# Kernel optimization log

Measured on AMD Instinct MI355X. Metric: run time of the kernel, lower is better.

Reference implementation:

```python
import jax, jax.numpy as jnp
import numpy as np

B, S, D, H, HD, E, DE = 2, 512, 768, 12, 64, 50, 50  # batch, seq, input_dim, heads, head_dim, edge_dim, dep_embed_dim


def setup_inputs() -> dict:
    key = jax.random.key(0)
    ks = jax.random.split(key, 16)
    def xn(k, shape, s=0.02):
        return (jax.random.normal(k, shape, jnp.float32) * s)
    return {
        'weight_prob_softmax': jax.random.uniform(ks[0], (B, S, S, E), jnp.float32),
        'weight_adj': jax.random.normal(ks[1], (B, S, S, E), jnp.float32),
        'gcn_inputs': jax.random.normal(ks[2], (B, S, D), jnp.float32),
        'self_loop': jax.random.uniform(ks[3], (B, S, S, E), jnp.float32),
        # self.linear
        'W_lin': xn(ks[4], (D, D)), 'b_lin': jnp.zeros((D,), jnp.float32),
        # additive attention vectors fc_w1 / fc_w2 (stored [H, HD])
        'fc_w1': xn(ks[5], (H, HD), 0.2), 'fc_w2': xn(ks[6], (H, HD), 0.2),
        # edge_mlp: Linear(E,128) -> ReLU -> (Dropout eval) -> Linear(128,H)
        'We1': xn(ks[7], (128, E), 0.1), 'be1': jnp.zeros((128,), jnp.float32),
        'We2': xn(ks[8], (H, 128), 0.1), 'be2': jnp.zeros((H,), jnp.float32),
        # self.W output projection
        'W_out': xn(ks[9], (D, D)), 'b_out': jnp.zeros((D,), jnp.float32),
        # LayerNorm params
        'ln_a': jnp.ones((D,), jnp.float32), 'ln_b': jnp.zeros((D,), jnp.float32),
        # highway.W split into column blocks: [edge | edge_i | edge_j | node1 | node2]
        'Wh_e': xn(ks[10], (DE, E), 0.1), 'Wh_ei': xn(ks[11], (DE, E), 0.1),
        'Wh_ej': xn(ks[12], (DE, E), 0.1), 'Wh_n1': xn(ks[13], (DE, D), 0.05),
        'Wh_n2': xn(ks[14], (DE, D), 0.05), 'bh': jnp.zeros((DE,), jnp.float32),
    }


def reference(weight_prob_softmax, weight_adj, gcn_inputs, self_loop,
              W_lin, b_lin, fc_w1, fc_w2, We1, be1, We2, be2,
              W_out, b_out, ln_a, ln_b, Wh_e, Wh_ei, Wh_ej, Wh_n1, Wh_n2, bh):
    wps = self_loop + weight_prob_softmax                      # [B,S,S,E]
    mask = jnp.sum(wps, axis=-1) == 0.0                        # [B,S,S]
    feature = (gcn_inputs @ W_lin.T + b_lin).reshape(B, S, H, HD)
    attn_src = jnp.einsum('bshd,hd->bhs', feature, fc_w1)      # [B,H,S]
    attn_dst = jnp.einsum('bshd,hd->bhs', feature, fc_w2)      # [B,H,S]
    # edge MLP bias (dropout is identity in eval)
    hmid = jax.nn.relu(jnp.einsum('bije,fe->bijf', wps, We1) + be1)  # [B,S,S,128]
    A = jnp.einsum('bijf,hf->bhij', hmid, We2) + be2[None, :, None, None]  # [B,H,S,S]
    attn = jax.nn.leaky_relu(attn_src[:, :, :, None] + attn_dst[:, :, None, :] + A,
                             negative_slope=0.01)
    attn = jnp.where(mask[:, None, :, :], -jnp.inf, attn)
    attn = jax.nn.softmax(attn, axis=-1)
    gcn = jnp.einsum('bhij,bjhd->bihd', attn, feature).reshape(B, S, D)
    gcn = gcn @ W_out.T + b_out
    # torch LayerNorm variant: unbiased std, divide by (std + eps)
    mean = jnp.mean(gcn, axis=-1, keepdims=True)
    std = jnp.std(gcn, axis=-1, ddof=1, keepdims=True)
    gcn = ln_a * (gcn - mean) / (std + 1e-6) + ln_b
    node = jax.nn.relu(gcn)                                    # [B,S,D]
    # RefiningStrategy: W([edge, edge_i, edge_j, node1, node2]) via block matmuls
    ediag = jnp.diagonal(weight_adj, axis1=1, axis2=2).transpose(0, 2, 1)  # [B,S,E]
    edge_out = (jnp.einsum('bije,fe->bijf', weight_adj, Wh_e)
                + (ediag @ Wh_ei.T)[:, :, None, :]             # edge_i[b,i,j]=diag[b,i]
                + (ediag @ Wh_ej.T)[:, None, :, :]             # edge_j[b,i,j]=diag[b,j]
                + (node @ Wh_n1.T)[:, None, :, :]              # node1[b,i,j]=node[b,j]
                + (node @ Wh_n2.T)[:, :, None, :]              # node2[b,i,j]=node[b,i]
                + bh)                                          # [B,S,S,DE]
    return node, edge_out
```

## Files before the change

kernel.cpp:

```cpp
#include <hip/hip_runtime.h>
#include <math.h>
#include <stddef.h>

#define BB 2
#define SS 512
#define DD 768
#define HH 12
#define HDIM 64
#define EE 50
#define DE 50
#define F1 128

typedef float f32x4 __attribute__((ext_vector_type(4)));
typedef short s16x8 __attribute__((ext_vector_type(8)));

static __device__ __forceinline__ unsigned short f2bf(float x) {
  unsigned int u = __float_as_uint(x);
  unsigned int r = u + 0x7fffu + ((u >> 16) & 1u);
  return (unsigned short)(r >> 16);
}
static __device__ __forceinline__ float bf2f(unsigned short b) {
  return __uint_as_float(((unsigned int)b) << 16);
}

__global__ __launch_bounds__(256) void k_gemm_bias(
    const float* __restrict__ X, int ldx,
    const float* __restrict__ W,
    const float* __restrict__ bias,
    float* __restrict__ Y, int ldy,
    int M, int N, int K)
{
  __shared__ float Xs[32][68];
  __shared__ float Ws[32][68];
  int t = threadIdx.x;
  int tx = t & 15, ty = t >> 4;
  int m0 = blockIdx.y * 64, n0 = blockIdx.x * 64;
  float acc[4][4] = {};
  for (int k0 = 0; k0 < K; k0 += 32) {
#pragma unroll
    for (int q = 0; q < 2; ++q) {
      int idx = t + q * 256;
      int r = idx >> 3, c = (idx & 7) << 2;
      float4 v = *(const float4*)(X + (size_t)(m0 + r) * ldx + k0 + c);
      Xs[c + 0][r] = v.x; Xs[c + 1][r] = v.y; Xs[c + 2][r] = v.z; Xs[c + 3][r] = v.w;
      float4 w = *(const float4*)(W + (size_t)(n0 + r) * K + k0 + c);
      Ws[c + 0][r] = w.x; Ws[c + 1][r] = w.y; Ws[c + 2][r] = w.z; Ws[c + 3][r] = w.w;
    }
    __syncthreads();
#pragma unroll
    for (int kk = 0; kk < 32; ++kk) {
      float a[4], b[4];
#pragma unroll
      for (int u = 0; u < 4; ++u) a[u] = Xs[kk][ty * 4 + u];
#pragma unroll
      for (int u = 0; u < 4; ++u) b[u] = Ws[kk][tx * 4 + u];
#pragma unroll
      for (int i = 0; i < 4; ++i)
#pragma unroll
        for (int j = 0; j < 4; ++j) acc[i][j] += a[i] * b[j];
    }
    __syncthreads();
  }
#pragma unroll
  for (int i = 0; i < 4; ++i) {
    int m = m0 + ty * 4 + i;
#pragma unroll
    for (int j = 0; j < 4; ++j) {
      int n = n0 + tx * 4 + j;
      Y[(size_t)m * ldy + n] = acc[i][j] + bias[n];
    }
  }
}

__global__ __launch_bounds__(192) void k_attnvec(
    const float* __restrict__ feat, const float* __restrict__ w1,
    const float* __restrict__ w2, float* __restrict__ src, float* __restrict__ dst)
{
  int bs = blockIdx.x;
  int t = threadIdx.x;
  int h = t >> 4, l = t & 15;
  float4 f = *(const float4*)(feat + (size_t)bs * DD + h * HDIM + l * 4);
  float4 a = *(const float4*)(w1 + h * HDIM + l * 4);
  float4 c = *(const float4*)(w2 + h * HDIM + l * 4);
  float ps = f.x * a.x + f.y * a.y + f.z * a.z + f.w * a.w;
  float pd = f.x * c.x + f.y * c.y + f.z * c.z + f.w * c.w;
#pragma unroll
  for (int o = 8; o > 0; o >>= 1) {
    ps += __shfl_xor(ps, o);
    pd += __shfl_xor(pd, o);
  }
  if (l == 0) {
    int b = bs >> 9, s = bs & 511;
    src[((b * HH + h) << 9) + s] = ps;
    dst[((b * HH + h) << 9) + s] = pd;
  }
}

__global__ __launch_bounds__(64) void k_prep(
    const float* __restrict__ We1, const float* __restrict__ be1,
    const float* __restrict__ We2, const float* __restrict__ Whe,
    s16x8* __restrict__ wtab, float* __restrict__ betab,
    s16x8* __restrict__ wtabE)
{
  const int l = threadIdx.x;
  const int lr = l & 15, lg = l >> 4;
#pragma unroll
  for (int ks = 0; ks < 2; ++ks)
#pragma unroll
    for (int n = 0; n < 8; ++n) {
      s16x8 v;
#pragma unroll
      for (int u = 0; u < 8; ++u) {
        int e = ks * 32 + lg * 8 + u;
        float x = (e < 50) ? We1[(n * 16 + lr) * 50 + e] : 0.0f;
        v[u] = (short)f2bf(x);
      }
      wtab[(ks * 8 + n) * 64 + l] = v;
    }
#pragma unroll
  for (int kk = 0; kk < 4; ++kk) {
    s16x8 v;
#pragma unroll
    for (int u = 0; u < 8; ++u) {
      int f = kk * 32 + lg * 8 + u;
      v[u] = (short)((lr < 12) ? f2bf(We2[lr * 128 + f]) : (unsigned short)0);
    }
    wtab[(16 + kk) * 64 + l] = v;
  }
#pragma unroll
  for (int n = 0; n < 8; ++n) betab[n * 64 + l] = be1[n * 16 + lr];
#pragma unroll
  for (int nt = 0; nt < 4; ++nt)
#pragma unroll
    for (int ks = 0; ks < 2; ++ks) {
      int f = nt * 16 + lr;
      s16x8 v;
#pragma unroll
      for (int u = 0; u < 8; ++u) {
        int e = ks * 32 + lg * 8 + u;
        float x = (f < 50 && e < 50) ? Whe[f * 50 + e] : 0.0f;
        v[u] = (short)f2bf(x);
      }
      wtabE[(nt * 2 + ks) * 64 + l] = v;
    }
}

__global__ __launch_bounds__(256, 4) void k_scores_mfma(
    const float* __restrict__ wprob, const float* __restrict__ sloop,
    const s16x8* __restrict__ wtab, const float* __restrict__ betab,
    const float* __restrict__ be2,
    const float* __restrict__ src, const float* __restrict__ dst,
    float* __restrict__ scores)
{
  __shared__ unsigned short wps_s[128][72];
  __shared__ unsigned short hmid_s[128][72];
  __shared__ float masks[128];

  const int blk = blockIdx.x;
  const int c = blk & 3;
  const int i = (blk >> 2) & 511;
  const int b = blk >> 11;
  const int j0c = c << 7;
  const int t = threadIdx.x;
  const int w = t >> 6, l = t & 63;
  const int lr = l & 15, lg = l >> 4;
  const int jbase = w * 32;

  const size_t rowbase = (size_t)(b * SS + i) * SS * EE + (size_t)c * 6400;
  float4 pw[7], psl[7];
  {
    const float* wp = wprob + rowbase;
    const float* sl = sloop + rowbase;
#pragma unroll
    for (int k = 0; k < 7; ++k)
      if (k < 6 || t < 64) {
        pw[k] = *(const float4*)(wp + 4 * (t + 256 * k));
        psl[k] = *(const float4*)(sl + 4 * (t + 256 * k));
      }
  }

  s16x8 wb[4];
#pragma unroll
  for (int kk = 0; kk < 4; ++kk) wb[kk] = wtab[(16 + kk) * 64 + l];
  float be1v[8];
#pragma unroll
  for (int n = 0; n < 8; ++n) be1v[n] = betab[n * 64 + l];
  const int hc = (lr < 12) ? lr : 0;
  const float be2v = be2[hc];
  const float srcv = src[((b * HH + hc) << 9) + i];
  const float* drow = dst + ((size_t)(b * HH + hc) << 9);
  float4 dv0 = *(const float4*)(drow + j0c + jbase + lg * 4);
  float4 dv1 = *(const float4*)(drow + j0c + jbase + 16 + lg * 4);

  for (int q = t; q < 896; q += 256) {
    int r = q / 7, cd = 25 + q % 7;
    ((unsigned int*)wps_s)[r * 36 + cd] = 0u;
  }

#pragma unroll
  for (int k = 0; k < 7; ++k)
    if (k < 6 || t < 64) {
      int f = 4 * (t + 256 * k);
      int j = f / 50;
      int e0 = f - j * 50;
      float vs[4] = {pw[k].x + psl[k].x, pw[k].y + psl[k].y,
                     pw[k].z + psl[k].z, pw[k].w + psl[k].w};
#pragma unroll
      for (int u = 0; u < 4; ++u) {
        int e = e0 + u, jj = j;
        if (e >= 50) { e -= 50; jj += 1; }
        wps_s[jj][e] = f2bf(vs[u]);
      }
    }
  __syncthreads();

  if (l < 32) {
    const unsigned short* row = wps_s[jbase + l];
    float s = 0.0f;
#pragma unroll
    for (int q = 0; q < 6; ++q) {
      s16x8 v = *(const s16x8*)(row + q * 8);
#pragma unroll
      for (int u = 0; u < 8; ++u) s += bf2f((unsigned short)v[u]);
    }
    unsigned int last = *(const unsigned int*)(row + 48);
    s += bf2f((unsigned short)(last & 0xffffu)) + bf2f((unsigned short)(last >> 16));
    masks[jbase + l] = (s == 0.0f) ? 1.0f : 0.0f;
  }

  s16x8 aA[2][2];
#pragma unroll
  for (int ks = 0; ks < 2; ++ks) {
    aA[0][ks] = *(const s16x8*)&wps_s[jbase + lr][ks * 32 + lg * 8];
    aA[1][ks] = *(const s16x8*)&wps_s[jbase + 16 + lr][ks * 32 + lg * 8];
  }

  f32x4 accB[2] = {};
#pragma unroll
  for (int h = 0; h < 2; ++h) {
    s16x8 wah[2][4];
#pragma unroll
    for (int ks = 0; ks < 2; ++ks)
#pragma unroll
      for (int nn = 0; nn < 4; ++nn)
        wah[ks][nn] = wtab[(ks * 8 + h * 4 + nn) * 64 + l];

    f32x4 accA[2][4] = {};
#pragma unroll
    for (int ks = 0; ks < 2; ++ks)
#pragma unroll
      for (int nn = 0; nn < 4; ++nn) {
        accA[0][nn] = __builtin_amdgcn_mfma_f32_16x16x32_bf16(aA[0][ks], wah[ks][nn], accA[0][nn], 0, 0, 0);
        accA[1][nn] = __builtin_amdgcn_mfma_f32_16x16x32_bf16(aA[1][ks], wah[ks][nn], accA[1][nn], 0, 0, 0);
      }
#pragma unroll
    for (int jt = 0; jt < 2; ++jt)
#pragma unroll
      for (int nn = 0; nn < 4; ++nn)
#pragma unroll
        for (int r = 0; r < 4; ++r) {
          float v = fmaxf(accA[jt][nn][r] + be1v[h * 4 + nn], 0.0f);
          hmid_s[jbase + jt * 16 + lg * 4 + r][nn * 16 + lr] = f2bf(v);
        }

#pragma unroll
    for (int kh = 0; kh < 2; ++kh) {
      int kk = 2 * h + kh;
      s16x8 a0 = *(const s16x8*)&hmid_s[jbase + lr][kh * 32 + lg * 8];
      s16x8 a1 = *(const s16x8*)&hmid_s[jbase + 16 + lr][kh * 32 + lg * 8];
      accB[0] = __builtin_amdgcn_mfma_f32_16x16x32_bf16(a0, wb[kk], accB[0], 0, 0, 0);
      accB[1] = __builtin_amdgcn_mfma_f32_16x16x32_bf16(a1, wb[kk], accB[1], 0, 0, 0);
    }
  }

  if (lr < 12) {
#pragma unroll
    for (int jt = 0; jt < 2; ++jt) {
      int jl = jbase + jt * 16 + lg * 4;
      const float4 dv = jt ? dv1 : dv0;
      float4 st;
#pragma unroll
      for (int r = 0; r < 4; ++r) {
        float x = accB[jt][r] + be2v + srcv + (&dv.x)[r];
        x = (x > 0.0f) ? x : 0.01f * x;
        if (masks[jl + r] != 0.0f) x = -INFINITY;
        (&st.x)[r] = x;
      }
      *(float4*)(scores + ((((size_t)(b * SS + i)) * HH + lr) << 9) + j0c + jl) = st;
    }
  }
}

__global__ __launch_bounds__(256) void k_softmax_pv(
    const float* __restrict__ scores, const float* __restrict__ feat,
    float* __restrict__ gout)
{
  __shared__ float p[2][12][512];
  int blk = blockIdx.x;
  int b = blk >> 8;
  int i0 = (blk & 255) << 1;
  int t = threadIdx.x;
  size_t base = ((size_t)(b * SS + i0) * HH) << 9;
  for (int q = t; q < 12288; q += 256) ((float*)p)[q] = scores[base + q];
  __syncthreads();

  int w = t >> 6, l = t & 63;
  for (int r = w; r < 24; r += 4) {
    int ii = r / 12, h = r % 12;
    float* row = p[ii][h];
    float vv[8];
    float m = -INFINITY;
#pragma unroll
    for (int u = 0; u < 8; ++u) {
      vv[u] = row[l + (u << 6)];
      m = fmaxf(m, vv[u]);
    }
#pragma unroll
    for (int o = 32; o > 0; o >>= 1) m = fmaxf(m, __shfl_xor(m, o));
    float s = 0.0f;
#pragma unroll
    for (int u = 0; u < 8; ++u) {
      float e = __expf(vv[u] - m);
      vv[u] = e;
      s += e;
    }
#pragma unroll
    for (int o = 32; o > 0; o >>= 1) s += __shfl_xor(s, o);
    float inv = 1.0f / s;
#pragma unroll
    for (int u = 0; u < 8; ++u) row[l + (u << 6)] = vv[u] * inv;
  }
  __syncthreads();

  float acc[2][3] = {};
  const float* fb = feat + (size_t)b * SS * DD;
  int h0 = t >> 6;
#pragma unroll 4
  for (int j = 0; j < 512; ++j) {
    const float* fr = fb + (size_t)j * DD;
    float f0 = fr[t], f1 = fr[t + 256], f2 = fr[t + 512];
    float p00 = p[0][h0][j], p10 = p[1][h0][j];
    float p01 = p[0][h0 + 4][j], p11 = p[1][h0 + 4][j];
    float p02 = p[0][h0 + 8][j], p12 = p[1][h0 + 8][j];
    acc[0][0] += p00 * f0; acc[0][1] += p01 * f1; acc[0][2] += p02 * f2;
    acc[1][0] += p10 * f0; acc[1][1] += p11 * f1; acc[1][2] += p12 * f2;
  }
#pragma unroll
  for (int ii = 0; ii < 2; ++ii)
#pragma unroll
    for (int u = 0; u < 3; ++u)
      gout[(size_t)(b * SS + i0 + ii) * DD + t + (u << 8)] = acc[ii][u];
}

__global__ __launch_bounds__(256) void k_ln(
    const float* __restrict__ gcn2, const float* __restrict__ ga,
    const float* __restrict__ gb, float* __restrict__ out)
{
  __shared__ float rs[4], rss[4];
  int row = blockIdx.x;
  int t = threadIdx.x;
  const float* x = gcn2 + (size_t)row * DD;
  float v[3];
  float s = 0.0f, ss2 = 0.0f;
#pragma unroll
  for (int u = 0; u < 3; ++u) {
    v[u] = x[t + (u << 8)];
    s += v[u];
    ss2 += v[u] * v[u];
  }
#pragma unroll
  for (int o = 32; o > 0; o >>= 1) {
    s += __shfl_down(s, o);
    ss2 += __shfl_down(ss2, o);
  }
  int w = t >> 6, l = t & 63;
  if (l == 0) { rs[w] = s; rss[w] = ss2; }
  __syncthreads();
  float S = rs[0] + rs[1] + rs[2] + rs[3];
  float SSum = rss[0] + rss[1] + rss[2] + rss[3];
  float mean = S * (1.0f / 768.0f);
  float var = (SSum - 768.0f * mean * mean) * (1.0f / 767.0f);
  var = fmaxf(var, 0.0f);
  float rinv = 1.0f / (sqrtf(var) + 1e-6f);
#pragma unroll
  for (int u = 0; u < 3; ++u) {
    int cidx = t + (u << 8);
    float y = ga[cidx] * (v[u] - mean) * rinv + gb[cidx];
    out[(size_t)row * DD + cidx] = fmaxf(y, 0.0f);
  }
}

__global__ __launch_bounds__(256) void k_pq(
    const float* __restrict__ node, const float* __restrict__ wadj,
    const float* __restrict__ Whei, const float* __restrict__ Whej,
    const float* __restrict__ Whn1, const float* __restrict__ Whn2,
    const float* __restrict__ bh, float* __restrict__ P, float* __restrict__ Q)
{
  __shared__ float nd[2][768];
  __shared__ float ed[2][64];
  const int bs0 = blockIdx.x * 2;
  const int t = threadIdx.x;
  const int w = t >> 6, l = t & 63;

  for (int q = t; q < 384; q += 256) {
    int rr = q / 192, idx = q % 192;
    *(float4*)(nd[rr] + idx * 4) =
        *(const float4*)(node + (size_t)(bs0 + rr) * DD + idx * 4);
  }
  {
    int rr = t >> 7, tt = t & 127;
    if (tt < 50) {
      int bs = bs0 + rr;
      int b = bs >> 9, s = bs & 511;
      ed[rr][tt] = wadj[((size_t)(b * SS + s) * SS + s) * EE + tt];
    }
  }
  __syncthreads();

  float4 n00 = *(const float4*)(nd[0] + l * 4);
  float4 n01 = *(const float4*)(nd[0] + 256 + l * 4);
  float4 n02 = *(const float4*)(nd[0] + 512 + l * 4);
  float4 n10 = *(const float4*)(nd[1] + l * 4);
  float4 n11 = *(const float4*)(nd[1] + 256 + l * 4);
  float4 n12 = *(const float4*)(nd[1] + 512 + l * 4);
  float el0 = (l < 50) ? ed[0][l] : 0.0f;
  float el1 = (l < 50) ? ed[1][l] : 0.0f;

  for (int o = w; o < 100; o += 4) {
    const int which = (o >= 50);
    const int f = o - which * 50;
    const float* Wn = which ? Whn1 : Whn2;
    const float* We = which ? Whej : Whei;
    const float* wr = Wn + f * DD;
    float4 w0 = *(const float4*)(wr + l * 4);
    float4 w1 = *(const float4*)(wr + 256 + l * 4);
    float4 w2 = *(const float4*)(wr + 512 + l * 4);
    float wev = (l < 50) ? We[f * EE + l] : 0.0f;
    float a0 = n00.x * w0.x + n00.y * w0.y + n00.z * w0.z + n00.w * w0.w
             + n01.x * w1.x + n01.y * w1.y + n01.z * w1.z + n01.w * w1.w
             + n02.x * w2.x + n02.y * w2.y + n02.z * w2.z + n02.w * w2.w
             + el0 * wev;
    float a1 = n10.x * w0.x + n10.y * w0.y + n10.z * w0.z + n10.w * w0.w
             + n11.x * w1.x + n11.y * w1.y + n11.z * w1.z + n11.w * w1.w
             + n12.x * w2.x + n12.y * w2.y + n12.z * w2.z + n12.w * w2.w
             + el1 * wev;
#pragma unroll
    for (int ofs = 32; ofs > 0; ofs >>= 1) {
      a0 += __shfl_xor(a0, ofs);
      a1 += __shfl_xor(a1, ofs);
    }
    if (l == 0) {
      float bias = which ? bh[f] : 0.0f;
      float* dst0 = (which ? Q : P) + (size_t)bs0 * DE + f;
      dst0[0] = a0 + bias;
      dst0[DE] = a1 + bias;
    }
  }
}

__global__ __launch_bounds__(256) void k_edge_mfma(
    const float* __restrict__ wadj, const s16x8* __restrict__ wtabE,
    const float* __restrict__ P, const float* __restrict__ Q,
    float* __restrict__ eout)
{
  __shared__ __align__(16) unsigned char raw[25600];
  unsigned short (*adj_s)[72] = (unsigned short(*)[72])raw;
  float* park = (float*)raw;
  __shared__ float P_s[64];

  const int t = threadIdx.x;
  const size_t n0 = (size_t)blockIdx.x * 128;
  const int b = (int)(n0 >> 18);
  const int i = (int)((n0 & 262143) >> 9);
  const int j0 = (int)(n0 & 511);
  const int w = t >> 6, l = t & 63;
  const int lr = l & 15, lg = l >> 4;
  const int mbase = w * 32;

  float4 pw[7];
  {
    const float* wp = wadj + n0 * EE;
#pragma unroll
    for (int k = 0; k < 7; ++k)
      if (k < 6 || t < 64) pw[k] = *(const float4*)(wp + 4 * (t + 256 * k));
  }

  s16x8 we[4][2];
#pragma unroll
  for (int nt = 0; nt < 4; ++nt)
#pragma unroll
    for (int ks = 0; ks < 2; ++ks) we[nt][ks] = wtabE[(nt * 2 + ks) * 64 + l];
  if (t < 64) P_s[t] = (t < 50) ? P[(size_t)(b * SS + i) * DE + t] : 0.0f;

  for (int q = t; q < 896; q += 256) {
    int r = q / 7, cd = 25 + q % 7;
    ((unsigned int*)adj_s)[r * 36 + cd] = 0u;
  }

#pragma unroll
  for (int k = 0; k < 7; ++k)
    if (k < 6 || t < 64) {
      int f = 4 * (t + 256 * k);
      int j = f / 50;
      int e0 = f - j * 50;
#pragma unroll
      for (int u = 0; u < 4; ++u) {
        int e = e0 + u, jj = j;
        if (e >= 50) { e -= 50; jj += 1; }
        adj_s[jj][e] = f2bf((&pw[k].x)[u]);
      }
    }
  __syncthreads();

  f32x4 acc[2][4] = {};
#pragma unroll
  for (int ks = 0; ks < 2; ++ks) {
    s16x8 a0 = *(const s16x8*)&adj_s[mbase + lr][ks * 32 + lg * 8];
    s16x8 a1 = *(const s16x8*)&adj_s[mbase + 16 + lr][ks * 32 + lg * 8];
#pragma unroll
    for (int nt = 0; nt < 4; ++nt) {
      acc[0][nt] = __builtin_amdgcn_mfma_f32_16x16x32_bf16(a0, we[nt][ks], acc[0][nt], 0, 0, 0);
      acc[1][nt] = __builtin_amdgcn_mfma_f32_16x16x32_bf16(a1, we[nt][ks], acc[1][nt], 0, 0, 0);
    }
  }
  __syncthreads();

#pragma unroll
  for (int nt = 0; nt < 4; ++nt) {
    int f = nt * 16 + lr;
    if (f < 50) {
      float pf = P_s[f];
#pragma unroll
      for (int mt = 0; mt < 2; ++mt) {
        int m = mbase + mt * 16 + lg * 4;
        const float* qp = Q + (size_t)(b * SS + j0 + m) * DE + f;
#pragma unroll
        for (int r = 0; r < 4; ++r)
          park[(m + r) * DE + f] = acc[mt][nt][r] + pf + qp[r * DE];
      }
    }
  }
  __syncthreads();

  const float4* s4 = (const float4*)park;
  float4* d4 = (float4*)(eout + n0 * DE);
  for (int q = t; q < 1600; q += 256) d4[q] = s4[q];
}

extern "C" void kernel_launch(void* const* d_in, const int* in_sizes, int n_in,
                              void* d_out, int out_size, void* d_ws, size_t ws_size,
                              hipStream_t stream)
{
  const float* wprob = (const float*)d_in[0];
  const float* wadj  = (const float*)d_in[1];
  const float* gin   = (const float*)d_in[2];
  const float* sloop = (const float*)d_in[3];
  const float* W_lin = (const float*)d_in[4];
  const float* b_lin = (const float*)d_in[5];
  const float* fw1   = (const float*)d_in[6];
  const float* fw2   = (const float*)d_in[7];
  const float* We1   = (const float*)d_in[8];
  const float* be1   = (const float*)d_in[9];
  const float* We2   = (const float*)d_in[10];
  const float* be2   = (const float*)d_in[11];
  const float* W_out = (const float*)d_in[12];
  const float* b_out = (const float*)d_in[13];
  const float* ln_a  = (const float*)d_in[14];
  const float* ln_b  = (const float*)d_in[15];
  const float* Whe   = (const float*)d_in[16];
  const float* Whei  = (const float*)d_in[17];
  const float* Whej  = (const float*)d_in[18];
  const float* Whn1  = (const float*)d_in[19];
  const float* Whn2  = (const float*)d_in[20];
  const float* bh    = (const float*)d_in[21];

  float* ws = (float*)d_ws;
  float* feature = ws + 0;
  float* src     = ws + 786432;
  float* dst     = ws + 798720;
  float* scores  = ws + 811008;
  float* gcnmid  = ws + 7102464;
  float* gcn2    = ws + 7888896;
  float* P       = ws + 8675328;
  float* Q       = ws + 8726528;
  s16x8* wtab    = (s16x8*)(ws + 8777728);
  float* betab   = ws + 8782848;
  s16x8* wtabE   = (s16x8*)(ws + 8783360);

  float* node = (float*)d_out;
  float* eout = (float*)d_out + 786432;

  k_prep<<<1, 64, 0, stream>>>(We1, be1, We2, Whe, wtab, betab, wtabE);
  k_gemm_bias<<<dim3(DD / 64, (BB * SS) / 64), 256, 0, stream>>>(
      gin, DD, W_lin, b_lin, feature, DD, BB * SS, DD, DD);
  k_attnvec<<<BB * SS, 192, 0, stream>>>(feature, fw1, fw2, src, dst);
  k_scores_mfma<<<BB * SS * 4, 256, 0, stream>>>(
      wprob, sloop, wtab, betab, be2, src, dst, scores);
  k_softmax_pv<<<BB * SS / 2, 256, 0, stream>>>(scores, feature, gcnmid);
  k_gemm_bias<<<dim3(DD / 64, (BB * SS) / 64), 256, 0, stream>>>(
      gcnmid, DD, W_out, b_out, gcn2, DD, BB * SS, DD, DD);
  k_ln<<<BB * SS, 256, 0, stream>>>(gcn2, ln_a, ln_b, node);
  k_pq<<<BB * SS / 2, 256, 0, stream>>>(node, wadj, Whei, Whej, Whn1, Whn2, bh, P, Q);
  k_edge_mfma<<<(BB * SS * SS) / 128, 256, 0, stream>>>(wadj, wtabE, P, Q, eout);
}
```

Baseline: 284.2 us.

## Split scores kernel into single-wave blocks with shared LDS buffer and no barrier

```diff
diff --git a/kernel.cpp b/kernel.cpp
--- a/kernel.cpp
+++ b/kernel.cpp
@@ -145,37 +145,34 @@
     }
 }
 
-__global__ __launch_bounds__(256, 4) void k_scores_mfma(
+__global__ __launch_bounds__(64, 6) void k_scores_mfma(
     const float* __restrict__ wprob, const float* __restrict__ sloop,
     const s16x8* __restrict__ wtab, const float* __restrict__ betab,
     const float* __restrict__ be2,
     const float* __restrict__ src, const float* __restrict__ dst,
     float* __restrict__ scores)
 {
-  __shared__ unsigned short wps_s[128][72];
-  __shared__ unsigned short hmid_s[128][72];
-  __shared__ float masks[128];
+  __shared__ unsigned short buf[32][72];
+  __shared__ float masks[32];
 
   const int blk = blockIdx.x;
-  const int c = blk & 3;
-  const int i = (blk >> 2) & 511;
-  const int b = blk >> 11;
-  const int j0c = c << 7;
-  const int t = threadIdx.x;
-  const int w = t >> 6, l = t & 63;
+  const int c = blk & 15;
+  const int i = (blk >> 4) & 511;
+  const int b = blk >> 13;
+  const int j0c = c << 5;
+  const int l = threadIdx.x;
   const int lr = l & 15, lg = l >> 4;
-  const int jbase = w * 32;
-
-  const size_t rowbase = (size_t)(b * SS + i) * SS * EE + (size_t)c * 6400;
+
+  const size_t rowbase = (size_t)(b * SS + i) * SS * EE + (size_t)c * 1600;
   float4 pw[7], psl[7];
   {
     const float* wp = wprob + rowbase;
     const float* sl = sloop + rowbase;
 #pragma unroll
     for (int k = 0; k < 7; ++k)
-      if (k < 6 || t < 64) {
-        pw[k] = *(const float4*)(wp + 4 * (t + 256 * k));
-        psl[k] = *(const float4*)(sl + 4 * (t + 256 * k));
+      if (k < 6 || l < 16) {
+        pw[k] = *(const float4*)(wp + 4 * (l + 64 * k));
+        psl[k] = *(const float4*)(sl + 4 * (l + 64 * k));
       }
   }
 
@@ -189,18 +186,18 @@
   const float be2v = be2[hc];
   const float srcv = src[((b * HH + hc) << 9) + i];
   const float* drow = dst + ((size_t)(b * HH + hc) << 9);
-  float4 dv0 = *(const float4*)(drow + j0c + jbase + lg * 4);
-  float4 dv1 = *(const float4*)(drow + j0c + jbase + 16 + lg * 4);
-
-  for (int q = t; q < 896; q += 256) {
+  float4 dv0 = *(const float4*)(drow + j0c + lg * 4);
+  float4 dv1 = *(const float4*)(drow + j0c + 16 + lg * 4);
+
+  for (int q = l; q < 224; q += 64) {
     int r = q / 7, cd = 25 + q % 7;
-    ((unsigned int*)wps_s)[r * 36 + cd] = 0u;
+    ((unsigned int*)buf)[r * 36 + cd] = 0u;
   }
 
 #pragma unroll
   for (int k = 0; k < 7; ++k)
-    if (k < 6 || t < 64) {
-      int f = 4 * (t + 256 * k);
+    if (k < 6 || l < 16) {
+      int f = 4 * (l + 64 * k);
       int j = f / 50;
       int e0 = f - j * 50;
       float vs[4] = {pw[k].x + psl[k].x, pw[k].y + psl[k].y,
@@ -209,30 +206,25 @@
       for (int u = 0; u < 4; ++u) {
         int e = e0 + u, jj = j;
         if (e >= 50) { e -= 50; jj += 1; }
-        wps_s[jj][e] = f2bf(vs[u]);
-      }
-    }
-  __syncthreads();
-
-  if (l < 32) {
-    const unsigned short* row = wps_s[jbase + l];
+        buf[jj][e] = f2bf(vs[u]);
+      }
+    }
+
+  {
+    int j = l & 31, half = l >> 5;
+    const unsigned short* row = buf[j] + half * 25;
     float s = 0.0f;
-#pragma unroll
-    for (int q = 0; q < 6; ++q) {
-      s16x8 v = *(const s16x8*)(row + q * 8);
-#pragma unroll
-      for (int u = 0; u < 8; ++u) s += bf2f((unsigned short)v[u]);
-    }
-    unsigned int last = *(const unsigned int*)(row + 48);
-    s += bf2f((unsigned short)(last & 0xffffu)) + bf2f((unsigned short)(last >> 16));
-    masks[jbase + l] = (s == 0.0f) ? 1.0f : 0.0f;
+#pragma unroll 5
+    for (int e = 0; e < 25; ++e) s += bf2f(row[e]);
+    s += __shfl_xor(s, 32);
+    if (l < 32) masks[j] = (s == 0.0f) ? 1.0f : 0.0f;
   }
 
   s16x8 aA[2][2];
 #pragma unroll
   for (int ks = 0; ks < 2; ++ks) {
-    aA[0][ks] = *(const s16x8*)&wps_s[jbase + lr][ks * 32 + lg * 8];
-    aA[1][ks] = *(const s16x8*)&wps_s[jbase + 16 + lr][ks * 32 + lg * 8];
+    aA[0][ks] = *(const s16x8*)&buf[lr][ks * 32 + lg * 8];
+    aA[1][ks] = *(const s16x8*)&buf[16 + lr][ks * 32 + lg * 8];
   }
 
   f32x4 accB[2] = {};
@@ -260,14 +252,14 @@
 #pragma unroll
         for (int r = 0; r < 4; ++r) {
           float v = fmaxf(accA[jt][nn][r] + be1v[h * 4 + nn], 0.0f);
-          hmid_s[jbase + jt * 16 + lg * 4 + r][nn * 16 + lr] = f2bf(v);
+          buf[jt * 16 + lg * 4 + r][nn * 16 + lr] = f2bf(v);
         }
 
 #pragma unroll
     for (int kh = 0; kh < 2; ++kh) {
       int kk = 2 * h + kh;
-      s16x8 a0 = *(const s16x8*)&hmid_s[jbase + lr][kh * 32 + lg * 8];
-      s16x8 a1 = *(const s16x8*)&hmid_s[jbase + 16 + lr][kh * 32 + lg * 8];
+      s16x8 a0 = *(const s16x8*)&buf[lr][kh * 32 + lg * 8];
+      s16x8 a1 = *(const s16x8*)&buf[16 + lr][kh * 32 + lg * 8];
       accB[0] = __builtin_amdgcn_mfma_f32_16x16x32_bf16(a0, wb[kk], accB[0], 0, 0, 0);
       accB[1] = __builtin_amdgcn_mfma_f32_16x16x32_bf16(a1, wb[kk], accB[1], 0, 0, 0);
     }
@@ -276,7 +268,7 @@
   if (lr < 12) {
 #pragma unroll
     for (int jt = 0; jt < 2; ++jt) {
-      int jl = jbase + jt * 16 + lg * 4;
+      int jl = jt * 16 + lg * 4;
       const float4 dv = jt ? dv1 : dv0;
       float4 st;
 #pragma unroll
@@ -594,7 +586,7 @@
   k_gemm_bias<<<dim3(DD / 64, (BB * SS) / 64), 256, 0, stream>>>(
       gin, DD, W_lin, b_lin, feature, DD, BB * SS, DD, DD);
   k_attnvec<<<BB * SS, 192, 0, stream>>>(feature, fw1, fw2, src, dst);
-  k_scores_mfma<<<BB * SS * 4, 256, 0, stream>>>(
+  k_scores_mfma<<<BB * SS * 16, 64, 0, stream>>>(
       wprob, sloop, wtab, betab, be2, src, dst, scores);
   k_softmax_pv<<<BB * SS / 2, 256, 0, stream>>>(scores, feature, gcnmid);
   k_gemm_bias<<<dim3(DD / 64, (BB * SS) / 64), 256, 0, stream>>>(
```

Result: slower. 325.2 us (+14.4%).
